# Kernel tuning notes

Hardware: AMD Instinct MI355X
Metric: run time of the kernel (lower is better)

Reference implementation:

```python
import jax, jax.numpy as jnp
import numpy as np

LEAKY_SLOPE = 0.01  # torch nn.LeakyReLU / F.leaky_relu default


def gcn_diffusion(adj, order, feat):
    # A_gcn = adj + I; sym-normalized diffusion D^-1/2 A D^-1/2 applied repeatedly
    B, N, _ = adj.shape
    A = adj + jnp.eye(N, dtype=adj.dtype)
    dinv_sqrt = jnp.sum(A, axis=2) ** -0.5  # [B, N]
    outs = []
    h = feat
    for _ in range(order):
        h = jnp.matmul(A, dinv_sqrt[..., None] * h) * dinv_sqrt[..., None]
        outs.append(h)
    return outs


def scattering_s4(adj, feat):
    # lazy random walk P = 1/2 (I + A D^-1); wavelets Psi_j = P^{2^{j-1}} - P^{2^j}
    dinv = 1.0 / jnp.sum(adj, axis=2)  # [B, N]
    p = feat
    us = []
    for _ in range(8):  # powers P^1 .. P^8
        p = 0.5 * p + 0.5 * jnp.matmul(adj, dinv[..., None] * p)
        us.append(p)
    h1 = feat - us[0]      # I - P
    h2 = us[0] - us[1]     # P - P^2
    h3 = us[1] - us[3]     # P^2 - P^4
    h4 = us[3] - us[7]     # P^4 - P^8
    return h1, h2, h3, h4


def sctconv(X, adj, W1, b1, W2, b2, a, moment):
    leaky = lambda x: jax.nn.leaky_relu(x, LEAKY_SLOPE)
    h = X  # [B, N, F]
    hA, hA2, hA3 = gcn_diffusion(adj, 3, X)
    hA, hA2, hA3 = leaky(hA), leaky(hA2), leaky(hA3)
    s1, s2, s3, s4 = scattering_s4(adj, X)
    mom = jnp.asarray(moment, dtype=X.dtype)
    s1 = jnp.abs(s1) ** mom
    s2 = jnp.abs(s2) ** mom
    s3 = jnp.abs(s3) ** mom
    s4 = jnp.abs(s4) ** mom
    # NOTE: original concatenates only (hA, hA2, s1..s4) -> 6 branches; hA3 is unused.
    h_all = jnp.stack([hA, hA2, s1, s2, s3, s4], axis=1)  # [B, 6, N, F]
    h_b = jnp.broadcast_to(h[:, None], h_all.shape)        # [B, 6, N, F]
    a_input = jnp.concatenate([h_b, h_all], axis=3)        # [B, 6, N, 2F]
    e = jnp.einsum('bknc,c->bkn', jax.nn.relu(a_input), a[:, 0])  # [B, 6, N]
    attention = jax.nn.softmax(e, axis=1)[..., None]       # [B, 6, N, 1]
    h_prime = jnp.mean(attention * h_all, axis=1)          # [B, N, F]
    out = leaky(h_prime @ W1.T + b1)
    out = leaky(out @ W2.T + b2)
    return out


def setup_inputs() -> dict:
    key = jax.random.key(0)
    kx, ka, k1, k2, k3, k4, k5 = jax.random.split(key, 7)
    B, N, F = 8, 4096, 64
    X = jax.random.normal(kx, (B, N, F), dtype=jnp.float32)
    adj = jax.random.uniform(ka, (B, N, N), dtype=jnp.float32)
    s = 1.0 / np.sqrt(F)
    W1 = jax.random.uniform(k1, (F, F), minval=-s, maxval=s, dtype=jnp.float32)
    b1 = jax.random.uniform(k2, (F,), minval=-s, maxval=s, dtype=jnp.float32)
    W2 = jax.random.uniform(k3, (F, F), minval=-s, maxval=s, dtype=jnp.float32)
    b2 = jax.random.uniform(k4, (F,), minval=-s, maxval=s, dtype=jnp.float32)
    a = jax.random.normal(k5, (2 * F, 1), dtype=jnp.float32) * 0.1
    return {"X": X, "adj": adj, "W1": W1, "b1": b1, "W2": W2, "b2": b2, "a": a, "moment": 1}


def reference(X, adj, W1, b1, W2, b2, a, moment):
    return sctconv(X, adj, W1, b1, W2, b2, a, moment)
```

## Files before the change

kernel.cpp:

```cpp
#include <hip/hip_runtime.h>
#include <hip/hip_bf16.h>
#include <cstdio>
#include <cstdint>

#define BB 8
#define NN 4096
#define FF 64

typedef __attribute__((ext_vector_type(8))) short bf16x8;
typedef __attribute__((ext_vector_type(4))) float f32x4;

__device__ __forceinline__ unsigned short f2bf(float f){
  unsigned int u = __float_as_uint(f);
  u += 0x7FFFu + ((u >> 16) & 1u);
  return (unsigned short)(u >> 16);
}

__device__ __forceinline__ float leaky01(float x){ return x > 0.f ? x : 0.01f * x; }

__global__ __launch_bounds__(256) void k_convert(const float* __restrict__ adj,
    unsigned short* __restrict__ adjb, float* __restrict__ dinv, float* __restrict__ dsq)
{
  size_t row = blockIdx.x;
  const float4* src = (const float4*)(adj + row * NN);
  ushort4* dst = (ushort4*)(adjb + row * NN);
  float s = 0.f;
  for (int i = threadIdx.x; i < NN / 4; i += 256){
    float4 v = src[i];
    s += (v.x + v.y) + (v.z + v.w);
    dst[i] = make_ushort4(f2bf(v.x), f2bf(v.y), f2bf(v.z), f2bf(v.w));
  }
  for (int o = 32; o; o >>= 1) s += __shfl_xor(s, o);
  __shared__ float red[4];
  if ((threadIdx.x & 63) == 0) red[threadIdx.x >> 6] = s;
  __syncthreads();
  if (threadIdx.x == 0){
    float t = (red[0] + red[1]) + (red[2] + red[3]);
    dinv[row] = 1.0f / t;
    dsq[row]  = 1.0f / sqrtf(t + 1.0f);
  }
}

__global__ __launch_bounds__(256) void k_prep(const float* __restrict__ X,
    const float* __restrict__ dinv, const float* __restrict__ dsq,
    unsigned short* __restrict__ vt)
{
  const int b = blockIdx.y, n0 = blockIdx.x * 64, tid = threadIdx.x;
  __shared__ unsigned short tg[64][65], ts[64][65];
  #pragma unroll
  for (int i = 0; i < 4; ++i){
    int idx = i * 256 + tid, n = idx >> 4, c4 = (idx & 15) * 4;
    size_t rb = (size_t)b * NN + n0 + n;
    float4 x = *(const float4*)(X + rb * 64 + c4);
    float di = dinv[b * NN + n0 + n], dv = dsq[b * NN + n0 + n];
    tg[c4 + 0][n] = f2bf(dv * x.x); tg[c4 + 1][n] = f2bf(dv * x.y);
    tg[c4 + 2][n] = f2bf(dv * x.z); tg[c4 + 3][n] = f2bf(dv * x.w);
    ts[c4 + 0][n] = f2bf(di * x.x); ts[c4 + 1][n] = f2bf(di * x.y);
    ts[c4 + 2][n] = f2bf(di * x.z); ts[c4 + 3][n] = f2bf(di * x.w);
  }
  __syncthreads();
  #pragma unroll
  for (int i = 0; i < 4; ++i){
    int idx = i * 256 + tid, c = idx >> 4, n4 = (idx & 15) * 4;
    *(ushort4*)(vt + ((size_t)b * 128 + c) * NN + n0 + n4) =
        make_ushort4(tg[c][n4], tg[c][n4 + 1], tg[c][n4 + 2], tg[c][n4 + 3]);
    *(ushort4*)(vt + ((size_t)b * 128 + 64 + c) * NN + n0 + n4) =
        make_ushort4(ts[c][n4], ts[c][n4 + 1], ts[c][n4 + 2], ts[c][n4 + 3]);
  }
}

template<int NC>
__global__ __launch_bounds__(256) void k_gemm(const unsigned short* __restrict__ adjb,
    const unsigned short* __restrict__ vt, float* __restrict__ Y, int c0)
{
  constexpr int NF = NC / 64;
  constexpr int BISS = NC / 32;
  __shared__ __align__(16) unsigned short As[2][64 * 64];
  __shared__ __align__(16) unsigned short Bs[2][NC * 64];
  const int b = blockIdx.y;
  const int m0 = blockIdx.x * 64;
  const int tid = threadIdx.x;
  const int w = tid >> 6, l = tid & 63;
  const unsigned short* Ag = adjb + (size_t)b * NN * NN;
  const unsigned short* Bg = vt + ((size_t)b * 128 + c0) * NN;

  auto stage = [&](int buf, int k0){
    #pragma unroll
    for (int i = 0; i < 2; ++i){
      int idx = i * 256 + tid, r = idx >> 3, g = idx & 7;
      const unsigned short* gp = Ag + (size_t)(m0 + r) * NN + k0 + ((g ^ (r & 7)) << 3);
      __builtin_amdgcn_global_load_lds((const __attribute__((address_space(1))) void*)gp,
          (__attribute__((address_space(3))) void*)(&As[buf][idx << 3]), 16, 0, 0);
    }
    #pragma unroll
    for (int i = 0; i < BISS; ++i){
      int idx = i * 256 + tid, c = idx >> 3, g = idx & 7;
      const unsigned short* gp = Bg + (size_t)c * NN + k0 + ((g ^ (c & 7)) << 3);
      __builtin_amdgcn_global_load_lds((const __attribute__((address_space(1))) void*)gp,
          (__attribute__((address_space(3))) void*)(&Bs[buf][idx << 3]), 16, 0, 0);
    }
  };

  f32x4 acc[4][NF];
  #pragma unroll
  for (int mi = 0; mi < 4; ++mi)
    #pragma unroll
    for (int ni = 0; ni < NF; ++ni)
      #pragma unroll
      for (int j = 0; j < 4; ++j) acc[mi][ni][j] = 0.f;

  stage(0, 0);
  const int r0 = l & 15, hq = l >> 4, sw = r0 & 7;
  constexpr int NT = NN / 64;
  for (int t = 0; t < NT; ++t){
    const int cur = t & 1;
    if (t + 1 < NT){
      stage(cur ^ 1, (t + 1) * 64);
      if constexpr (NC == 128) asm volatile("s_waitcnt vmcnt(6)" ::: "memory");
      else                     asm volatile("s_waitcnt vmcnt(4)" ::: "memory");
    } else {
      asm volatile("s_waitcnt vmcnt(0)" ::: "memory");
    }
    __builtin_amdgcn_s_barrier();
    asm volatile("" ::: "memory");
    #pragma unroll
    for (int kk = 0; kk < 2; ++kk){
      const int g8 = ((kk * 4 + hq) ^ sw) << 3;
      bf16x8 af[4], bfr[NF];
      #pragma unroll
      for (int mi = 0; mi < 4; ++mi)
        af[mi] = *(const bf16x8*)&As[cur][(mi * 16 + r0) * 64 + g8];
      #pragma unroll
      for (int ni = 0; ni < NF; ++ni)
        bfr[ni] = *(const bf16x8*)&Bs[cur][(w * 16 * NF + ni * 16 + r0) * 64 + g8];
      #pragma unroll
      for (int mi = 0; mi < 4; ++mi)
        #pragma unroll
        for (int ni = 0; ni < NF; ++ni)
          acc[mi][ni] = __builtin_amdgcn_mfma_f32_16x16x32_bf16(af[mi], bfr[ni], acc[mi][ni], 0, 0, 0);
    }
    asm volatile("" ::: "memory");
    __builtin_amdgcn_s_barrier();
    asm volatile("" ::: "memory");
  }
  #pragma unroll
  for (int mi = 0; mi < 4; ++mi)
    #pragma unroll
    for (int ni = 0; ni < NF; ++ni)
      #pragma unroll
      for (int j = 0; j < 4; ++j){
        int row = m0 + mi * 16 + hq * 4 + j;
        int col = c0 + w * 16 * NF + ni * 16 + r0;
        Y[((size_t)b * NN + row) * 128 + col] = acc[mi][ni][j];
      }
}

__global__ __launch_bounds__(256) void k_epi(const float* __restrict__ Y,
    const float* __restrict__ sprev, float* __restrict__ P, float* __restrict__ snap,
    const float* __restrict__ dinv, const float* __restrict__ dsq,
    const float* __restrict__ gprev, float* __restrict__ gout,
    unsigned short* __restrict__ vt, int writeGcnVt)
{
  const int b = blockIdx.y, n0 = blockIdx.x * 64, tid = threadIdx.x;
  __shared__ unsigned short vts[64][65];
  __shared__ unsigned short vtg[64][65];
  const bool doG = (gprev != nullptr);
  #pragma unroll
  for (int i = 0; i < 4; ++i){
    int idx = i * 256 + tid, n = idx >> 4, c4 = (idx & 15) * 4;
    size_t rb = (size_t)b * NN + n0 + n;
    float4 y  = *(const float4*)(Y + rb * 128 + 64 + c4);
    float4 pv = *(const float4*)(sprev + rb * 64 + c4);
    float4 pn = { 0.5f * (pv.x + y.x), 0.5f * (pv.y + y.y),
                  0.5f * (pv.z + y.z), 0.5f * (pv.w + y.w) };
    *(float4*)(P + rb * 64 + c4) = pn;
    if (snap) *(float4*)(snap + rb * 64 + c4) = pn;
    float di = dinv[b * NN + n0 + n];
    vts[c4 + 0][n] = f2bf(di * pn.x); vts[c4 + 1][n] = f2bf(di * pn.y);
    vts[c4 + 2][n] = f2bf(di * pn.z); vts[c4 + 3][n] = f2bf(di * pn.w);
  }
  if (doG){
    #pragma unroll
    for (int i = 0; i < 4; ++i){
      int idx = i * 256 + tid, n = idx >> 4, c4 = (idx & 15) * 4;
      size_t rb = (size_t)b * NN + n0 + n;
      float4 y  = *(const float4*)(Y + rb * 128 + c4);
      float4 hv = *(const float4*)(gprev + rb * 64 + c4);
      float dv = dsq[b * NN + n0 + n];
      float4 hn = { (y.x + dv * hv.x) * dv, (y.y + dv * hv.y) * dv,
                    (y.z + dv * hv.z) * dv, (y.w + dv * hv.w) * dv };
      *(float4*)(gout + rb * 64 + c4) = hn;
      if (writeGcnVt){
        vtg[c4 + 0][n] = f2bf(dv * hn.x); vtg[c4 + 1][n] = f2bf(dv * hn.y);
        vtg[c4 + 2][n] = f2bf(dv * hn.z); vtg[c4 + 3][n] = f2bf(dv * hn.w);
      }
    }
  }
  __syncthreads();
  if (vt){
    #pragma unroll
    for (int i = 0; i < 4; ++i){
      int idx = i * 256 + tid, c = idx >> 4, n4 = (idx & 15) * 4;
      *(ushort4*)(vt + ((size_t)b * 128 + 64 + c) * NN + n0 + n4) =
          make_ushort4(vts[c][n4], vts[c][n4 + 1], vts[c][n4 + 2], vts[c][n4 + 3]);
    }
    if (doG && writeGcnVt){
      #pragma unroll
      for (int i = 0; i < 4; ++i){
        int idx = i * 256 + tid, c = idx >> 4, n4 = (idx & 15) * 4;
        *(ushort4*)(vt + ((size_t)b * 128 + c) * NN + n0 + n4) =
            make_ushort4(vtg[c][n4], vtg[c][n4 + 1], vtg[c][n4 + 2], vtg[c][n4 + 3]);
      }
    }
  }
}

__global__ __launch_bounds__(256) void k_attn(
    const float* __restrict__ X,  const float* __restrict__ hA, const float* __restrict__ hA2,
    const float* __restrict__ U1, const float* __restrict__ U2, const float* __restrict__ U4,
    const float* __restrict__ U8, const float* __restrict__ W1, const float* __restrict__ b1,
    const float* __restrict__ W2, const float* __restrict__ b2, const float* __restrict__ av,
    const int* __restrict__ momp, float* __restrict__ out)
{
  __shared__ float W1s[64][65], W2s[64][65];
  __shared__ float a1s[64], a2s[64], b1s[64], b2s[64];
  __shared__ float hp[4][64], o1[4][64];
  const int tid = threadIdx.x;
  for (int e = tid; e < 4096; e += 256){
    W1s[e >> 6][e & 63] = W1[e];
    W2s[e >> 6][e & 63] = W2[e];
  }
  if (tid < 64){ a1s[tid] = av[tid]; a2s[tid] = av[64 + tid]; b1s[tid] = b1[tid]; b2s[tid] = b2[tid]; }
  __syncthreads();
  const int w = tid >> 6, l = tid & 63;
  size_t row = (size_t)blockIdx.x * 4 + w;
  size_t off = row * 64 + l;
  float x  = X[off];
  float u1 = U1[off], u2 = U2[off], u4 = U4[off], u8 = U8[off];
  float br[6];
  br[0] = leaky01(hA[off]);
  br[1] = leaky01(hA2[off]);
  float d1 = fabsf(x - u1), d2 = fabsf(u1 - u2), d3 = fabsf(u2 - u4), d4 = fabsf(u4 - u8);
  int mom = *momp;
  if (mom == 1){ br[2] = d1; br[3] = d2; br[4] = d3; br[5] = d4; }
  else {
    float m = (float)mom;
    br[2] = powf(d1, m); br[3] = powf(d2, m); br[4] = powf(d3, m); br[5] = powf(d4, m);
  }
  float v = fmaxf(x, 0.f) * a1s[l];
  for (int o = 32; o; o >>= 1) v += __shfl_xor(v, o);
  float base = v;
  float e[6];
  #pragma unroll
  for (int k = 0; k < 6; ++k){
    float t = fmaxf(br[k], 0.f) * a2s[l];
    for (int o = 32; o; o >>= 1) t += __shfl_xor(t, o);
    e[k] = base + t;
  }
  float mx = e[0];
  #pragma unroll
  for (int k = 1; k < 6; ++k) mx = fmaxf(mx, e[k]);
  float s = 0.f, att[6];
  #pragma unroll
  for (int k = 0; k < 6; ++k){ att[k] = expf(e[k] - mx); s += att[k]; }
  float inv = 1.0f / (6.0f * s);
  float hpv = 0.f;
  #pragma unroll
  for (int k = 0; k < 6; ++k) hpv += att[k] * br[k];
  hpv *= inv;
  hp[w][l] = hpv;
  __syncthreads();
  float acc = b1s[l];
  #pragma unroll 8
  for (int c = 0; c < 64; ++c) acc += hp[w][c] * W1s[l][c];
  o1[w][l] = leaky01(acc);
  __syncthreads();
  float acc2 = b2s[l];
  #pragma unroll 8
  for (int c = 0; c < 64; ++c) acc2 += o1[w][c] * W2s[l][c];
  out[off] = leaky01(acc2);
}

static constexpr size_t OFF_ADJB = 0;
static constexpr size_t OFF_VT   = OFF_ADJB + (size_t)BB * NN * NN * 2;
static constexpr size_t OFF_Y    = OFF_VT   + (size_t)BB * 128 * NN * 2;
static constexpr size_t OFF_HA   = OFF_Y    + (size_t)BB * NN * 128 * 4;
static constexpr size_t OFF_HA2  = OFF_HA   + (size_t)BB * NN * 64 * 4;
static constexpr size_t OFF_P    = OFF_HA2  + (size_t)BB * NN * 64 * 4;
static constexpr size_t OFF_U1   = OFF_P    + (size_t)BB * NN * 64 * 4;
static constexpr size_t OFF_U2   = OFF_U1   + (size_t)BB * NN * 64 * 4;
static constexpr size_t OFF_U4   = OFF_U2   + (size_t)BB * NN * 64 * 4;
static constexpr size_t OFF_U8   = OFF_U4   + (size_t)BB * NN * 64 * 4;
static constexpr size_t OFF_DINV = OFF_U8   + (size_t)BB * NN * 64 * 4;
static constexpr size_t OFF_DS   = OFF_DINV + (size_t)BB * NN * 4;
static constexpr size_t WS_NEED  = OFF_DS   + (size_t)BB * NN * 4;

extern "C" void kernel_launch(void* const* d_in, const int* in_sizes, int n_in,
                              void* d_out, int out_size, void* d_ws, size_t ws_size,
                              hipStream_t stream)
{
  const float* X   = (const float*)d_in[0];
  const float* adj = (const float*)d_in[1];
  const float* W1  = (const float*)d_in[2];
  const float* b1  = (const float*)d_in[3];
  const float* W2  = (const float*)d_in[4];
  const float* b2  = (const float*)d_in[5];
  const float* av  = (const float*)d_in[6];
  const int*  momp = (const int*)d_in[7];
  float* out = (float*)d_out;

  if (ws_size < WS_NEED){
    fprintf(stderr, "kernel_launch: workspace too small: %zu < %zu\n", ws_size, WS_NEED);
    return;
  }
  char* w = (char*)d_ws;
  unsigned short* adjb = (unsigned short*)(w + OFF_ADJB);
  unsigned short* vt   = (unsigned short*)(w + OFF_VT);
  float* Y    = (float*)(w + OFF_Y);
  float* hA   = (float*)(w + OFF_HA);
  float* hA2  = (float*)(w + OFF_HA2);
  float* P    = (float*)(w + OFF_P);
  float* U1   = (float*)(w + OFF_U1);
  float* U2   = (float*)(w + OFF_U2);
  float* U4   = (float*)(w + OFF_U4);
  float* U8   = (float*)(w + OFF_U8);
  float* dinv = (float*)(w + OFF_DINV);
  float* dsq  = (float*)(w + OFF_DS);

  k_convert<<<BB * NN, 256, 0, stream>>>(adj, adjb, dinv, dsq);
  dim3 tg(NN / 64, BB);
  k_prep<<<tg, 256, 0, stream>>>(X, dinv, dsq, vt);

  k_gemm<128><<<tg, 256, 0, stream>>>(adjb, vt, Y, 0);
  k_epi<<<tg, 256, 0, stream>>>(Y, X, P, U1, dinv, dsq, X, hA, vt, 1);
  k_gemm<128><<<tg, 256, 0, stream>>>(adjb, vt, Y, 0);
  k_epi<<<tg, 256, 0, stream>>>(Y, P, P, U2, dinv, dsq, hA, hA2, vt, 0);
  for (int k = 3; k <= 8; ++k){
    k_gemm<64><<<tg, 256, 0, stream>>>(adjb, vt, Y, 64);
    float* snap = (k == 4) ? U4 : (k == 8) ? U8 : nullptr;
    unsigned short* vtn = (k < 8) ? vt : nullptr;
    k_epi<<<tg, 256, 0, stream>>>(Y, P, P, snap, dinv, dsq, nullptr, nullptr, vtn, 0);
  }

  k_attn<<<BB * NN / 4, 256, 0, stream>>>(X, hA, hA2, U1, U2, U4, U8,
                                          W1, b1, W2, b2, av, momp, out);
}
```

Before: 839.0 us.

## Fuse diffusion epilogue into GEMM, halve M tile, ping-pong vt buffers

Moves the per-step elementwise epilogue (lazy-walk update, GCN normalization, snapshot, bf16 transposed operand write) into the GEMM kernel. This removes the fp32 Y intermediate and the separate epilogue launches. The M tile shrinks from 64 to 32 rows for more blocks and occupancy. The vt operand is double-buffered so blocks can write the next operand while other blocks still read the current one. The trade-offs are more B-tile traffic per output row and uncoalesced strided epilogue stores.

After: 832.6 us. About the same (-0.8%).

```diff
diff --git a/kernel.cpp b/kernel.cpp
--- a/kernel.cpp
+++ b/kernel.cpp
@@ -70,30 +70,35 @@
 }
 
 template<int NC>
-__global__ __launch_bounds__(256) void k_gemm(const unsigned short* __restrict__ adjb,
-    const unsigned short* __restrict__ vt, float* __restrict__ Y, int c0)
+__global__ __launch_bounds__(256, 4) void k_gemm_fused(
+    const unsigned short* __restrict__ adjb,
+    const unsigned short* __restrict__ vtR, int c0,
+    const float* __restrict__ sprev, float* __restrict__ P, float* __restrict__ snap,
+    const float* __restrict__ dinv, int writeVtS,
+    const float* __restrict__ gprev, float* __restrict__ gout,
+    const float* __restrict__ dsq, int writeVtG,
+    unsigned short* __restrict__ vtW)
 {
   constexpr int NF = NC / 64;
-  constexpr int BISS = NC / 32;
-  __shared__ __align__(16) unsigned short As[2][64 * 64];
+  constexpr int BI = NC / 32;
+  __shared__ __align__(16) unsigned short As[2][32 * 64];
   __shared__ __align__(16) unsigned short Bs[2][NC * 64];
   const int b = blockIdx.y;
-  const int m0 = blockIdx.x * 64;
+  const int m0 = blockIdx.x * 32;
   const int tid = threadIdx.x;
   const int w = tid >> 6, l = tid & 63;
   const unsigned short* Ag = adjb + (size_t)b * NN * NN;
-  const unsigned short* Bg = vt + ((size_t)b * 128 + c0) * NN;
+  const unsigned short* Bg = vtR + ((size_t)b * 128 + c0) * NN;
 
   auto stage = [&](int buf, int k0){
-    #pragma unroll
-    for (int i = 0; i < 2; ++i){
-      int idx = i * 256 + tid, r = idx >> 3, g = idx & 7;
+    {
+      int r = tid >> 3, g = tid & 7;
       const unsigned short* gp = Ag + (size_t)(m0 + r) * NN + k0 + ((g ^ (r & 7)) << 3);
       __builtin_amdgcn_global_load_lds((const __attribute__((address_space(1))) void*)gp,
-          (__attribute__((address_space(3))) void*)(&As[buf][idx << 3]), 16, 0, 0);
+          (__attribute__((address_space(3))) void*)(&As[buf][tid << 3]), 16, 0, 0);
     }
     #pragma unroll
-    for (int i = 0; i < BISS; ++i){
+    for (int i = 0; i < BI; ++i){
       int idx = i * 256 + tid, c = idx >> 3, g = idx & 7;
       const unsigned short* gp = Bg + (size_t)c * NN + k0 + ((g ^ (c & 7)) << 3);
       __builtin_amdgcn_global_load_lds((const __attribute__((address_space(1))) void*)gp,
@@ -101,9 +106,9 @@
     }
   };
 
-  f32x4 acc[4][NF];
-  #pragma unroll
-  for (int mi = 0; mi < 4; ++mi)
+  f32x4 acc[2][NF];
+  #pragma unroll
+  for (int mi = 0; mi < 2; ++mi)
     #pragma unroll
     for (int ni = 0; ni < NF; ++ni)
       #pragma unroll
@@ -116,8 +121,8 @@
     const int cur = t & 1;
     if (t + 1 < NT){
       stage(cur ^ 1, (t + 1) * 64);
-      if constexpr (NC == 128) asm volatile("s_waitcnt vmcnt(6)" ::: "memory");
-      else                     asm volatile("s_waitcnt vmcnt(4)" ::: "memory");
+      if constexpr (NC == 128) asm volatile("s_waitcnt vmcnt(5)" ::: "memory");
+      else                     asm volatile("s_waitcnt vmcnt(3)" ::: "memory");
     } else {
       asm volatile("s_waitcnt vmcnt(0)" ::: "memory");
     }
@@ -126,15 +131,15 @@
     #pragma unroll
     for (int kk = 0; kk < 2; ++kk){
       const int g8 = ((kk * 4 + hq) ^ sw) << 3;
-      bf16x8 af[4], bfr[NF];
-      #pragma unroll
-      for (int mi = 0; mi < 4; ++mi)
+      bf16x8 af[2], bfr[NF];
+      #pragma unroll
+      for (int mi = 0; mi < 2; ++mi)
         af[mi] = *(const bf16x8*)&As[cur][(mi * 16 + r0) * 64 + g8];
       #pragma unroll
       for (int ni = 0; ni < NF; ++ni)
         bfr[ni] = *(const bf16x8*)&Bs[cur][(w * 16 * NF + ni * 16 + r0) * 64 + g8];
       #pragma unroll
-      for (int mi = 0; mi < 4; ++mi)
+      for (int mi = 0; mi < 2; ++mi)
         #pragma unroll
         for (int ni = 0; ni < NF; ++ni)
           acc[mi][ni] = __builtin_amdgcn_mfma_f32_16x16x32_bf16(af[mi], bfr[ni], acc[mi][ni], 0, 0, 0);
@@ -143,73 +148,61 @@
     __builtin_amdgcn_s_barrier();
     asm volatile("" ::: "memory");
   }
-  #pragma unroll
-  for (int mi = 0; mi < 4; ++mi)
+
+  const bool isScat = (NC == 64) || (w >= 2);
+  if (isScat){
+    const int wS = (NC == 64) ? w : (w - 2);
     #pragma unroll
-    for (int ni = 0; ni < NF; ++ni)
-      #pragma unroll
-      for (int j = 0; j < 4; ++j){
-        int row = m0 + mi * 16 + hq * 4 + j;
-        int col = c0 + w * 16 * NF + ni * 16 + r0;
-        Y[((size_t)b * NN + row) * 128 + col] = acc[mi][ni][j];
+    for (int mi = 0; mi < 2; ++mi){
+      const int rb = m0 + mi * 16 + hq * 4;
+      const size_t rowb = (size_t)b * NN + rb;
+      float4 dv4 = *(const float4*)(dinv + (size_t)b * NN + rb);
+      #pragma unroll
+      for (int ni = 0; ni < NF; ++ni){
+        const int cs = wS * 16 * NF + ni * 16 + r0;
+        float pn[4];
+        #pragma unroll
+        for (int j = 0; j < 4; ++j){
+          float pv = sprev[(rowb + j) * 64 + cs];
+          pn[j] = 0.5f * (pv + acc[mi][ni][j]);
+          P[(rowb + j) * 64 + cs] = pn[j];
+        }
+        if (snap){
+          #pragma unroll
+          for (int j = 0; j < 4; ++j) snap[(rowb + j) * 64 + cs] = pn[j];
+        }
+        if (writeVtS){
+          ushort4 vv = make_ushort4(f2bf(dv4.x * pn[0]), f2bf(dv4.y * pn[1]),
+                                    f2bf(dv4.z * pn[2]), f2bf(dv4.w * pn[3]));
+          *(ushort4*)(vtW + ((size_t)b * 128 + 64 + cs) * NN + rb) = vv;
+        }
       }
-}
-
-__global__ __launch_bounds__(256) void k_epi(const float* __restrict__ Y,
-    const float* __restrict__ sprev, float* __restrict__ P, float* __restrict__ snap,
-    const float* __restrict__ dinv, const float* __restrict__ dsq,
-    const float* __restrict__ gprev, float* __restrict__ gout,
-    unsigned short* __restrict__ vt, int writeGcnVt)
-{
-  const int b = blockIdx.y, n0 = blockIdx.x * 64, tid = threadIdx.x;
-  __shared__ unsigned short vts[64][65];
-  __shared__ unsigned short vtg[64][65];
-  const bool doG = (gprev != nullptr);
-  #pragma unroll
-  for (int i = 0; i < 4; ++i){
-    int idx = i * 256 + tid, n = idx >> 4, c4 = (idx & 15) * 4;
-    size_t rb = (size_t)b * NN + n0 + n;
-    float4 y  = *(const float4*)(Y + rb * 128 + 64 + c4);
-    float4 pv = *(const float4*)(sprev + rb * 64 + c4);
-    float4 pn = { 0.5f * (pv.x + y.x), 0.5f * (pv.y + y.y),
-                  0.5f * (pv.z + y.z), 0.5f * (pv.w + y.w) };
-    *(float4*)(P + rb * 64 + c4) = pn;
-    if (snap) *(float4*)(snap + rb * 64 + c4) = pn;
-    float di = dinv[b * NN + n0 + n];
-    vts[c4 + 0][n] = f2bf(di * pn.x); vts[c4 + 1][n] = f2bf(di * pn.y);
-    vts[c4 + 2][n] = f2bf(di * pn.z); vts[c4 + 3][n] = f2bf(di * pn.w);
-  }
-  if (doG){
-    #pragma unroll
-    for (int i = 0; i < 4; ++i){
-      int idx = i * 256 + tid, n = idx >> 4, c4 = (idx & 15) * 4;
-      size_t rb = (size_t)b * NN + n0 + n;
-      float4 y  = *(const float4*)(Y + rb * 128 + c4);
-      float4 hv = *(const float4*)(gprev + rb * 64 + c4);
-      float dv = dsq[b * NN + n0 + n];
-      float4 hn = { (y.x + dv * hv.x) * dv, (y.y + dv * hv.y) * dv,
-                    (y.z + dv * hv.z) * dv, (y.w + dv * hv.w) * dv };
-      *(float4*)(gout + rb * 64 + c4) = hn;
-      if (writeGcnVt){
-        vtg[c4 + 0][n] = f2bf(dv * hn.x); vtg[c4 + 1][n] = f2bf(dv * hn.y);
-        vtg[c4 + 2][n] = f2bf(dv * hn.z); vtg[c4 + 3][n] = f2bf(dv * hn.w);
-      }
-    }
-  }
-  __syncthreads();
-  if (vt){
-    #pragma unroll
-    for (int i = 0; i < 4; ++i){
-      int idx = i * 256 + tid, c = idx >> 4, n4 = (idx & 15) * 4;
-      *(ushort4*)(vt + ((size_t)b * 128 + 64 + c) * NN + n0 + n4) =
-          make_ushort4(vts[c][n4], vts[c][n4 + 1], vts[c][n4 + 2], vts[c][n4 + 3]);
-    }
-    if (doG && writeGcnVt){
-      #pragma unroll
-      for (int i = 0; i < 4; ++i){
-        int idx = i * 256 + tid, c = idx >> 4, n4 = (idx & 15) * 4;
-        *(ushort4*)(vt + ((size_t)b * 128 + c) * NN + n0 + n4) =
-            make_ushort4(vtg[c][n4], vtg[c][n4 + 1], vtg[c][n4 + 2], vtg[c][n4 + 3]);
+    }
+  }
+  if constexpr (NC == 128){
+    if (!isScat){
+      #pragma unroll
+      for (int mi = 0; mi < 2; ++mi){
+        const int rb = m0 + mi * 16 + hq * 4;
+        const size_t rowb = (size_t)b * NN + rb;
+        float4 dq4 = *(const float4*)(dsq + (size_t)b * NN + rb);
+        #pragma unroll
+        for (int ni = 0; ni < NF; ++ni){
+          const int cg = w * 16 * NF + ni * 16 + r0;
+          float hn[4];
+          const float dq[4] = {dq4.x, dq4.y, dq4.z, dq4.w};
+          #pragma unroll
+          for (int j = 0; j < 4; ++j){
+            float hv = gprev[(rowb + j) * 64 + cg];
+            hn[j] = (acc[mi][ni][j] + dq[j] * hv) * dq[j];
+            gout[(rowb + j) * 64 + cg] = hn[j];
+          }
+          if (writeVtG){
+            ushort4 vv = make_ushort4(f2bf(dq[0] * hn[0]), f2bf(dq[1] * hn[1]),
+                                      f2bf(dq[2] * hn[2]), f2bf(dq[3] * hn[3]));
+            *(ushort4*)(vtW + ((size_t)b * 128 + cg) * NN + rb) = vv;
+          }
+        }
       }
     }
   }
@@ -282,9 +275,9 @@
 }
 
 static constexpr size_t OFF_ADJB = 0;
-static constexpr size_t OFF_VT   = OFF_ADJB + (size_t)BB * NN * NN * 2;
-static constexpr size_t OFF_Y    = OFF_VT   + (size_t)BB * 128 * NN * 2;
-static constexpr size_t OFF_HA   = OFF_Y    + (size_t)BB * NN * 128 * 4;
+static constexpr size_t OFF_VTA  = OFF_ADJB + (size_t)BB * NN * NN * 2;
+static constexpr size_t OFF_VTB  = OFF_VTA  + (size_t)BB * 128 * NN * 2;
+static constexpr size_t OFF_HA   = OFF_VTB  + (size_t)BB * 128 * NN * 2;
 static constexpr size_t OFF_HA2  = OFF_HA   + (size_t)BB * NN * 64 * 4;
 static constexpr size_t OFF_P    = OFF_HA2  + (size_t)BB * NN * 64 * 4;
 static constexpr size_t OFF_U1   = OFF_P    + (size_t)BB * NN * 64 * 4;
@@ -315,8 +308,8 @@
   }
   char* w = (char*)d_ws;
   unsigned short* adjb = (unsigned short*)(w + OFF_ADJB);
-  unsigned short* vt   = (unsigned short*)(w + OFF_VT);
-  float* Y    = (float*)(w + OFF_Y);
+  unsigned short* vtA  = (unsigned short*)(w + OFF_VTA);
+  unsigned short* vtB  = (unsigned short*)(w + OFF_VTB);
   float* hA   = (float*)(w + OFF_HA);
   float* hA2  = (float*)(w + OFF_HA2);
   float* P    = (float*)(w + OFF_P);
@@ -328,18 +321,23 @@
   float* dsq  = (float*)(w + OFF_DS);
 
   k_convert<<<BB * NN, 256, 0, stream>>>(adj, adjb, dinv, dsq);
-  dim3 tg(NN / 64, BB);
-  k_prep<<<tg, 256, 0, stream>>>(X, dinv, dsq, vt);
-
-  k_gemm<128><<<tg, 256, 0, stream>>>(adjb, vt, Y, 0);
-  k_epi<<<tg, 256, 0, stream>>>(Y, X, P, U1, dinv, dsq, X, hA, vt, 1);
-  k_gemm<128><<<tg, 256, 0, stream>>>(adjb, vt, Y, 0);
-  k_epi<<<tg, 256, 0, stream>>>(Y, P, P, U2, dinv, dsq, hA, hA2, vt, 0);
+  dim3 tg64(NN / 64, BB);
+  k_prep<<<tg64, 256, 0, stream>>>(X, dinv, dsq, vtA);
+
+  dim3 gg(NN / 32, BB);
+  k_gemm_fused<128><<<gg, 256, 0, stream>>>(adjb, vtA, 0,
+      X, P, U1, dinv, 1, X, hA, dsq, 1, vtB);
+  k_gemm_fused<128><<<gg, 256, 0, stream>>>(adjb, vtB, 0,
+      P, P, U2, dinv, 1, hA, hA2, dsq, 0, vtA);
+  unsigned short* vr = vtA;
+  unsigned short* vw = vtB;
   for (int k = 3; k <= 8; ++k){
-    k_gemm<64><<<tg, 256, 0, stream>>>(adjb, vt, Y, 64);
-    float* snap = (k == 4) ? U4 : (k == 8) ? U8 : nullptr;
-    unsigned short* vtn = (k < 8) ? vt : nullptr;
-    k_epi<<<tg, 256, 0, stream>>>(Y, P, P, snap, dinv, dsq, nullptr, nullptr, vtn, 0);
+    float* snap = (k == 4) ? U4 : (k == 8) ? nullptr : nullptr;
+    float* pdst = (k == 8) ? U8 : P;
+    if (k == 4) snap = U4;
+    k_gemm_fused<64><<<gg, 256, 0, stream>>>(adjb, vr, 64,
+        P, pdst, snap, dinv, (k < 8) ? 1 : 0, nullptr, nullptr, nullptr, 0, vw);
+    unsigned short* t = vr; vr = vw; vw = t;
   }
 
   k_attn<<<BB * NN / 4, 256, 0, stream>>>(X, hA, hA2, U1, U2, U4, U8,
```
